# Optimization experiments

Measured on AMD Instinct MI355X. Metric: run time of the kernel, lower is better.

## Reference

```python
import jax, jax.numpy as jnp
import numpy as np

D_MODEL = 512
D_STATE = 16
D_CONV = 5
EXPAND = 2
HEADDIM = 64
D_INNER = EXPAND * D_MODEL            # 1024
NHEADS = D_INNER // HEADDIM           # 16
NGROUPS = 1
CONV_DIM = D_INNER + 2 * NGROUPS * D_STATE          # 1056
D_IN_PROJ = 2 * D_INNER + 2 * NGROUPS * D_STATE + NHEADS  # 2096
B_SZ, SEQ = 16, 960
EPS = 1e-5


def _mamba_params(key):
    ks = jax.random.split(key, 5)
    return dict(
        W_in=jax.random.normal(ks[0], (D_MODEL, D_IN_PROJ), jnp.float32) * 0.02,
        conv_w=jax.random.normal(ks[1], (CONV_DIM, D_CONV), jnp.float32) * 0.1,
        conv_b=jnp.zeros((CONV_DIM,), jnp.float32),
        dt_bias=jnp.log(jnp.expm1(jax.random.uniform(ks[2], (NHEADS,), jnp.float32, 0.001, 0.1))),
        A_log=jnp.log(jax.random.uniform(ks[3], (NHEADS,), jnp.float32, 1.0, 16.0)),
        D=jnp.ones((NHEADS,), jnp.float32),
        norm_w=jnp.ones((D_INNER,), jnp.float32),
        W_out=jax.random.normal(ks[4], (D_INNER, D_MODEL), jnp.float32) * 0.02,
    )


def setup_inputs() -> dict:
    key = jax.random.key(0)
    kx, kf, kb, kp = jax.random.split(key, 4)
    inp = {"x": jax.random.normal(kx, (B_SZ, SEQ, D_MODEL), jnp.float32)}
    for pref, k in (("fwd_", kf), ("bwd_", kb)):
        for n, v in _mamba_params(k).items():
            inp[pref + n] = v
    kp1, kp2 = jax.random.split(kp)
    inp["proj_W"] = jax.random.normal(kp1, (2 * D_MODEL, D_MODEL), jnp.float32) * 0.02
    inp["proj_b"] = jnp.zeros((D_MODEL,), jnp.float32)
    inp["ln_g"] = jnp.ones((D_MODEL,), jnp.float32)
    inp["ln_b"] = jnp.zeros((D_MODEL,), jnp.float32)
    return inp


def _mamba2(x, W_in, conv_w, conv_b, dt_bias, A_log, D, norm_w, W_out):
    """Mamba-2 block (mamba_ssm semantics): in_proj -> causal depthwise conv
    + silu -> selective SSM scan -> gated RMSNorm -> out_proj."""
    B, L, _ = x.shape
    zxbcdt = x @ W_in                                  # (B,L,2096)
    z = zxbcdt[..., :D_INNER]
    xBC = zxbcdt[..., D_INNER:D_INNER + CONV_DIM]
    dt = jax.nn.softplus(zxbcdt[..., D_INNER + CONV_DIM:] + dt_bias)  # (B,L,H)
    # causal depthwise conv over time
    xp = jnp.pad(xBC, ((0, 0), (D_CONV - 1, 0), (0, 0))).transpose(0, 2, 1)  # (B,C,Lp)
    xc = jax.lax.conv_general_dilated(
        xp, conv_w[:, None, :], window_strides=(1,), padding='VALID',
        dimension_numbers=('NCH', 'OIH', 'NCH'),
        feature_group_count=CONV_DIM).transpose(0, 2, 1)                  # (B,L,C)
    xBC = jax.nn.silu(xc + conv_b)
    xs = xBC[..., :D_INNER].reshape(B, L, NHEADS, HEADDIM)                # (B,L,H,P)
    Bm = xBC[..., D_INNER:D_INNER + D_STATE]                              # (B,L,N)
    Cm = xBC[..., D_INNER + D_STATE:]                                     # (B,L,N)
    A = -jnp.exp(A_log)                                                   # (H,)
    dA = jnp.exp(dt * A)                                                  # (B,L,H)
    dtx = dt[..., None] * xs                                              # (B,L,H,P)

    def step(h, inp):
        dA_t, dtx_t, B_t, C_t = inp
        # h: (B,H,P,N)
        h = h * dA_t[:, :, None, None] + jnp.einsum('bhp,bn->bhpn', dtx_t, B_t)
        y = jnp.einsum('bhpn,bn->bhp', h, C_t)
        return h, y

    h0 = jnp.zeros((B, NHEADS, HEADDIM, D_STATE), x.dtype)
    _, ys = jax.lax.scan(
        step, h0,
        (dA.transpose(1, 0, 2), dtx.transpose(1, 0, 2, 3),
         Bm.transpose(1, 0, 2), Cm.transpose(1, 0, 2)))
    y = ys.transpose(1, 0, 2, 3) + D[None, None, :, None] * xs            # (B,L,H,P)
    y = y.reshape(B, L, D_INNER)
    # gated RMSNorm (norm_before_gate=False)
    y = y * jax.nn.silu(z)
    y = y * jax.lax.rsqrt(jnp.mean(y * y, axis=-1, keepdims=True) + EPS) * norm_w
    return y @ W_out


def reference(x,
              fwd_W_in, fwd_conv_w, fwd_conv_b, fwd_dt_bias, fwd_A_log, fwd_D, fwd_norm_w, fwd_W_out,
              bwd_W_in, bwd_conv_w, bwd_conv_b, bwd_dt_bias, bwd_A_log, bwd_D, bwd_norm_w, bwd_W_out,
              proj_W, proj_b, ln_g, ln_b):
    x_f = _mamba2(x, fwd_W_in, fwd_conv_w, fwd_conv_b, fwd_dt_bias, fwd_A_log, fwd_D, fwd_norm_w, fwd_W_out)
    x_b = jnp.flip(_mamba2(jnp.flip(x, 1), bwd_W_in, bwd_conv_w, bwd_conv_b, bwd_dt_bias, bwd_A_log, bwd_D, bwd_norm_w, bwd_W_out), 1)
    x_out = jnp.concatenate([x_f, x_b], axis=-1) @ proj_W + proj_b
    h = x + x_out  # dropout is identity in eval
    mu = jnp.mean(h, axis=-1, keepdims=True)
    var = jnp.mean((h - mu) ** 2, axis=-1, keepdims=True)
    return (h - mu) * jax.lax.rsqrt(var + EPS) * ln_g + ln_b
```

## Files before the change

kernel.cpp:

```cpp
#include <hip/hip_runtime.h>
#include <hip/hip_bf16.h>

#define D_MODEL   512
#define D_STATE   16
#define D_CONV    5
#define HEADDIM   64
#define D_INNER   1024
#define NHEADS    16
#define CONV_DIM  1056
#define D_IN_PROJ 2096
#define B_SZ      16
#define SEQ       960
#define MROWS     (B_SZ*SEQ)
#define EPS       1e-5f
#define NCHUNK    6
#define CLEN      160

typedef __attribute__((ext_vector_type(8))) short   short8;
typedef __attribute__((ext_vector_type(8))) ushort  u16x8;
typedef __attribute__((ext_vector_type(4))) float   f32x4;

__device__ __forceinline__ ushort bf16_rne(float f) {
  union { float f; unsigned u; } x; x.f = f;
  unsigned u = x.u;
  return (ushort)((u + 0x7FFFu + ((u >> 16) & 1u)) >> 16);
}
__device__ __forceinline__ float bf16_f(ushort h) {
  union { unsigned u; float f; } x; x.u = ((unsigned)h) << 16;
  return x.f;
}
__device__ __forceinline__ void cvt_split(float v, ushort& h, ushort& l) {
  h = bf16_rne(v);
  l = bf16_rne(v - bf16_f(h));
}

#define LDK 40

__global__ __launch_bounds__(256) void gemm_mfma(
    const float* __restrict__ A, const float* __restrict__ Bt,
    float* __restrict__ C, const float* __restrict__ bias,
    int M, int N, int K, int lda, int ldb, int ldc, int accum)
{
  __shared__ ushort As_hi[128][LDK], As_lo[128][LDK];
  __shared__ ushort Bs_hi[128][LDK], Bs_lo[128][LDK];

  const int tid  = threadIdx.x;
  const int lane = tid & 63;
  const int wave = tid >> 6;
  const int wm   = wave >> 1;
  const int wn   = wave & 1;
  const int brow = blockIdx.x * 128;
  const int bcol = blockIdx.y * 128;

  const int sr = tid >> 1;
  const int sq = (tid & 1) * 16;

  f32x4 acc[4][4];
  #pragma unroll
  for (int i = 0; i < 4; ++i)
    #pragma unroll
    for (int j = 0; j < 4; ++j) acc[i][j] = f32x4{0.f, 0.f, 0.f, 0.f};

  const int fr = lane & 15;
  const int fk = (lane >> 4) * 8;

#define CS(F, HV, LV, I) { ushort th_, tl_; cvt_split((F), th_, tl_); HV[I] = th_; LV[I] = tl_; }

  for (int k0 = 0; k0 < K; k0 += 32) {
    {
      const float* s = &A[(size_t)(brow + sr) * lda + k0 + sq];
      float4 a0 = *(const float4*)(s);
      float4 a1 = *(const float4*)(s + 4);
      float4 a2 = *(const float4*)(s + 8);
      float4 a3 = *(const float4*)(s + 12);
      u16x8 h0, h1, l0, l1;
      CS(a0.x, h0, l0, 0) CS(a0.y, h0, l0, 1) CS(a0.z, h0, l0, 2) CS(a0.w, h0, l0, 3)
      CS(a1.x, h0, l0, 4) CS(a1.y, h0, l0, 5) CS(a1.z, h0, l0, 6) CS(a1.w, h0, l0, 7)
      CS(a2.x, h1, l1, 0) CS(a2.y, h1, l1, 1) CS(a2.z, h1, l1, 2) CS(a2.w, h1, l1, 3)
      CS(a3.x, h1, l1, 4) CS(a3.y, h1, l1, 5) CS(a3.z, h1, l1, 6) CS(a3.w, h1, l1, 7)
      *(u16x8*)&As_hi[sr][sq]     = h0;
      *(u16x8*)&As_hi[sr][sq + 8] = h1;
      *(u16x8*)&As_lo[sr][sq]     = l0;
      *(u16x8*)&As_lo[sr][sq + 8] = l1;
    }
    {
      int n = bcol + sr;
      u16x8 h0 = {0,0,0,0,0,0,0,0}, h1 = h0, l0 = h0, l1 = h0;
      if (n < N) {
        const float* s = &Bt[(size_t)n * ldb + k0 + sq];
        float4 b0 = *(const float4*)(s);
        float4 b1 = *(const float4*)(s + 4);
        float4 b2 = *(const float4*)(s + 8);
        float4 b3 = *(const float4*)(s + 12);
        CS(b0.x, h0, l0, 0) CS(b0.y, h0, l0, 1) CS(b0.z, h0, l0, 2) CS(b0.w, h0, l0, 3)
        CS(b1.x, h0, l0, 4) CS(b1.y, h0, l0, 5) CS(b1.z, h0, l0, 6) CS(b1.w, h0, l0, 7)
        CS(b2.x, h1, l1, 0) CS(b2.y, h1, l1, 1) CS(b2.z, h1, l1, 2) CS(b2.w, h1, l1, 3)
        CS(b3.x, h1, l1, 4) CS(b3.y, h1, l1, 5) CS(b3.z, h1, l1, 6) CS(b3.w, h1, l1, 7)
      }
      *(u16x8*)&Bs_hi[sr][sq]     = h0;
      *(u16x8*)&Bs_hi[sr][sq + 8] = h1;
      *(u16x8*)&Bs_lo[sr][sq]     = l0;
      *(u16x8*)&Bs_lo[sr][sq + 8] = l1;
    }
    __syncthreads();

    short8 ah[4], al[4], bh[4], bl[4];
    #pragma unroll
    for (int mf = 0; mf < 4; ++mf) {
      int r = wm * 64 + mf * 16 + fr;
      ah[mf] = *(const short8*)&As_hi[r][fk];
      al[mf] = *(const short8*)&As_lo[r][fk];
    }
    #pragma unroll
    for (int nf = 0; nf < 4; ++nf) {
      int n = wn * 64 + nf * 16 + fr;
      bh[nf] = *(const short8*)&Bs_hi[n][fk];
      bl[nf] = *(const short8*)&Bs_lo[n][fk];
    }
    #pragma unroll
    for (int mf = 0; mf < 4; ++mf)
      #pragma unroll
      for (int nf = 0; nf < 4; ++nf) {
        acc[mf][nf] = __builtin_amdgcn_mfma_f32_16x16x32_bf16(ah[mf], bh[nf], acc[mf][nf], 0, 0, 0);
        acc[mf][nf] = __builtin_amdgcn_mfma_f32_16x16x32_bf16(ah[mf], bl[nf], acc[mf][nf], 0, 0, 0);
        acc[mf][nf] = __builtin_amdgcn_mfma_f32_16x16x32_bf16(al[mf], bh[nf], acc[mf][nf], 0, 0, 0);
      }
    __syncthreads();
  }
#undef CS

  const int orow0 = brow + wm * 64 + ((lane >> 4) << 2);
  const int ocol0 = bcol + wn * 64 + fr;
  #pragma unroll
  for (int nf = 0; nf < 4; ++nf) {
    int col = ocol0 + nf * 16;
    if (col < N) {
      float bv = bias ? bias[col] : 0.f;
      #pragma unroll
      for (int mf = 0; mf < 4; ++mf) {
        #pragma unroll
        for (int j = 0; j < 4; ++j) {
          size_t idx = (size_t)(orow0 + mf * 16 + j) * ldc + col;
          float v = acc[mf][nf][j] + bv;
          if (accum) v += C[idx];
          C[idx] = v;
        }
      }
    }
  }
}

__global__ __launch_bounds__(256) void transpose_f32(
    const float* __restrict__ in, float* __restrict__ out, int R, int C)
{
  __shared__ float t[32][33];
  int c0 = blockIdx.x * 32, r0 = blockIdx.y * 32;
  int tx = threadIdx.x & 31, ty = threadIdx.x >> 5;
  #pragma unroll
  for (int i = 0; i < 32; i += 8) {
    int r = r0 + ty + i, c = c0 + tx;
    t[ty + i][tx] = (r < R && c < C) ? in[(size_t)r * C + c] : 0.f;
  }
  __syncthreads();
  #pragma unroll
  for (int i = 0; i < 32; i += 8) {
    int c = c0 + ty + i, r = r0 + tx;
    if (c < C && r < R) out[(size_t)c * R + r] = t[tx][ty + i];
  }
}

#define BM 128
#define BN 128
#define BKK 16

__global__ __launch_bounds__(256) void gemm_f32(
    const float* __restrict__ A, const float* __restrict__ B,
    float* __restrict__ C, const float* __restrict__ bias,
    int N, int K, int lda, int ldb, int ldc, int accum)
{
  __shared__ float As[BKK][BM + 4];
  __shared__ float Bs[BKK][BN + 4];

  const int tid = threadIdx.x;
  const int bm = blockIdx.x * BM;
  const int bn = blockIdx.y * BN;
  const int tx = tid & 15;
  const int ty = tid >> 4;

  const int am = tid >> 2;
  const int ak = (tid & 3) * 4;
  const int bk = tid >> 5;
  const int bc = (tid & 31) * 4;

  float acc[8][8];
  #pragma unroll
  for (int i = 0; i < 8; ++i)
    #pragma unroll
    for (int j = 0; j < 8; ++j) acc[i][j] = 0.f;

  const int colb = bn + bc;
  const bool bok = (colb < N);

  for (int k0 = 0; k0 < K; k0 += BKK) {
    float4 av0 = *(const float4*)&A[(size_t)(bm + am) * lda + k0 + ak];
    float4 av1 = *(const float4*)&A[(size_t)(bm + am + 64) * lda + k0 + ak];
    As[ak + 0][am]      = av0.x; As[ak + 1][am]      = av0.y;
    As[ak + 2][am]      = av0.z; As[ak + 3][am]      = av0.w;
    As[ak + 0][am + 64] = av1.x; As[ak + 1][am + 64] = av1.y;
    As[ak + 2][am + 64] = av1.z; As[ak + 3][am + 64] = av1.w;
    float4 z4 = make_float4(0.f, 0.f, 0.f, 0.f);
    float4 bv0 = bok ? *(const float4*)&B[(size_t)(k0 + bk) * ldb + colb]     : z4;
    float4 bv1 = bok ? *(const float4*)&B[(size_t)(k0 + bk + 8) * ldb + colb] : z4;
    *(float4*)&Bs[bk][bc]     = bv0;
    *(float4*)&Bs[bk + 8][bc] = bv1;
    __syncthreads();

    #pragma unroll
    for (int k = 0; k < BKK; ++k) {
      float4 a0 = *(const float4*)&As[k][ty * 4];
      float4 a1 = *(const float4*)&As[k][64 + ty * 4];
      float4 b0 = *(const float4*)&Bs[k][tx * 4];
      float4 b1 = *(const float4*)&Bs[k][64 + tx * 4];
      float a[8] = {a0.x, a0.y, a0.z, a0.w, a1.x, a1.y, a1.z, a1.w};
      float bb[8] = {b0.x, b0.y, b0.z, b0.w, b1.x, b1.y, b1.z, b1.w};
      #pragma unroll
      for (int i = 0; i < 8; ++i)
        #pragma unroll
        for (int j = 0; j < 8; ++j)
          acc[i][j] = __builtin_fmaf(a[i], bb[j], acc[i][j]);
    }
    __syncthreads();
  }

  const int n0 = bn + tx * 4;
  const int n1 = bn + 64 + tx * 4;
  float4 bias0 = make_float4(0.f, 0.f, 0.f, 0.f), bias1 = bias0;
  if (bias) {
    if (n0 < N) bias0 = *(const float4*)&bias[n0];
    if (n1 < N) bias1 = *(const float4*)&bias[n1];
  }
  #pragma unroll
  for (int i = 0; i < 8; ++i) {
    int row = bm + ((i < 4) ? (ty * 4 + i) : (64 + ty * 4 + i - 4));
    if (n0 < N) {
      float4 v = make_float4(acc[i][0] + bias0.x, acc[i][1] + bias0.y,
                             acc[i][2] + bias0.z, acc[i][3] + bias0.w);
      if (accum) {
        float4 c = *(const float4*)&C[(size_t)row * ldc + n0];
        v.x += c.x; v.y += c.y; v.z += c.z; v.w += c.w;
      }
      *(float4*)&C[(size_t)row * ldc + n0] = v;
    }
    if (n1 < N) {
      float4 v = make_float4(acc[i][4] + bias1.x, acc[i][5] + bias1.y,
                             acc[i][6] + bias1.z, acc[i][7] + bias1.w);
      if (accum) {
        float4 c = *(const float4*)&C[(size_t)row * ldc + n1];
        v.x += c.x; v.y += c.y; v.z += c.z; v.w += c.w;
      }
      *(float4*)&C[(size_t)row * ldc + n1] = v;
    }
  }
}

__global__ __launch_bounds__(256) void conv_silu(
    const float* __restrict__ zx, const float* __restrict__ cw,
    const float* __restrict__ cb, float* __restrict__ out, int dir)
{
  int idx = blockIdx.x * 256 + threadIdx.x;
  if (idx >= MROWS * CONV_DIM) return;
  int c  = idx % CONV_DIM;
  int bl = idx / CONV_DIM;
  int l  = bl % SEQ;
  int rowbase = bl - l;

  float acc = 0.f;
  #pragma unroll
  for (int j = 0; j < D_CONV; ++j) {
    int li = dir ? (l + 4 - j) : (l - 4 + j);
    if (li >= 0 && li < SEQ)
      acc = __builtin_fmaf(cw[c * D_CONV + j],
                           zx[(size_t)(rowbase + li) * D_IN_PROJ + D_INNER + c], acc);
  }
  float v = acc + cb[c];
  out[idx] = v / (1.f + __expf(-v));
}

__global__ __launch_bounds__(64) void scan_pass1(
    const float* __restrict__ zx, const float* __restrict__ xc,
    const float* __restrict__ dtb_p, const float* __restrict__ Alog_p,
    float* __restrict__ states, float* __restrict__ Pbuf, int dir)
{
  int blk = blockIdx.x;
  int c   = blk % NCHUNK;
  int bh  = blk / NCHUNK;
  int b = bh >> 4, hd = bh & 15;
  float dtb = dtb_p[hd];
  float A   = -__expf(Alog_p[hd]);
  int p = threadIdx.x;
  const float* xrow = xc + (size_t)b * SEQ * CONV_DIM;
  const float* zrow = zx + (size_t)b * SEQ * D_IN_PROJ;

  float h[16];
  #pragma unroll
  for (int n = 0; n < 16; ++n) h[n] = 0.f;
  float P = 1.f;

  const int s0 = c * CLEN, s1 = s0 + CLEN;

  float xv0, dtr0; float4 B0[4];
  float xv1, dtr1; float4 B1[4];

#define P1LOAD(ss, XV, DTR, BB) do {                                        \
    int tt_ = dir ? (SEQ - 1 - (ss)) : (ss);                                \
    size_t xb_ = (size_t)tt_ * CONV_DIM;                                    \
    XV  = xrow[xb_ + hd * 64 + p];                                          \
    DTR = zrow[(size_t)tt_ * D_IN_PROJ + (D_INNER + CONV_DIM) + hd];        \
    const float4* B4_ = (const float4*)(xrow + xb_ + D_INNER);              \
    BB[0] = B4_[0]; BB[1] = B4_[1]; BB[2] = B4_[2]; BB[3] = B4_[3];         \
  } while (0)

  P1LOAD(s0, xv0, dtr0, B0);
  P1LOAD(s0 + 1, xv1, dtr1, B1);

  #pragma unroll 4
  for (int s = s0; s < s1; ++s) {
    float dtrb = dtr0 + dtb;
    float dt = (dtrb > 20.f) ? dtrb : log1pf(__expf(dtrb));
    float dA = __expf(dt * A);
    P *= dA;
    float dtx = dt * xv0;
#define ST1(n, Bc) h[n] = __builtin_fmaf(h[n], dA, dtx * (Bc));
    ST1(0,  B0[0].x) ST1(1,  B0[0].y) ST1(2,  B0[0].z) ST1(3,  B0[0].w)
    ST1(4,  B0[1].x) ST1(5,  B0[1].y) ST1(6,  B0[1].z) ST1(7,  B0[1].w)
    ST1(8,  B0[2].x) ST1(9,  B0[2].y) ST1(10, B0[2].z) ST1(11, B0[2].w)
    ST1(12, B0[3].x) ST1(13, B0[3].y) ST1(14, B0[3].z) ST1(15, B0[3].w)
#undef ST1
    xv0 = xv1; dtr0 = dtr1;
    #pragma unroll
    for (int q = 0; q < 4; ++q) B0[q] = B1[q];
    int sn = s + 2; if (sn > s1 - 1) sn = s1 - 1;
    P1LOAD(sn, xv1, dtr1, B1);
  }
#undef P1LOAD

  float4* sp = (float4*)&states[(((size_t)bh * NCHUNK + c) * 64 + p) * 16];
  sp[0] = make_float4(h[0],  h[1],  h[2],  h[3]);
  sp[1] = make_float4(h[4],  h[5],  h[6],  h[7]);
  sp[2] = make_float4(h[8],  h[9],  h[10], h[11]);
  sp[3] = make_float4(h[12], h[13], h[14], h[15]);
  if (p == 0) Pbuf[bh * NCHUNK + c] = P;
}

__global__ __launch_bounds__(64) void scan_combine(
    float* __restrict__ states, const float* __restrict__ Pbuf)
{
  int bh = blockIdx.x;
  int p  = threadIdx.x;
  float4 h0 = make_float4(0,0,0,0), h1 = h0, h2 = h0, h3 = h0;
  for (int c = 0; c < NCHUNK; ++c) {
    float4* sp = (float4*)&states[(((size_t)bh * NCHUNK + c) * 64 + p) * 16];
    float P = Pbuf[bh * NCHUNK + c];
    float4 s0 = sp[0], s1 = sp[1], s2 = sp[2], s3 = sp[3];
    sp[0] = h0; sp[1] = h1; sp[2] = h2; sp[3] = h3;
    h0.x = __builtin_fmaf(P, h0.x, s0.x); h0.y = __builtin_fmaf(P, h0.y, s0.y);
    h0.z = __builtin_fmaf(P, h0.z, s0.z); h0.w = __builtin_fmaf(P, h0.w, s0.w);
    h1.x = __builtin_fmaf(P, h1.x, s1.x); h1.y = __builtin_fmaf(P, h1.y, s1.y);
    h1.z = __builtin_fmaf(P, h1.z, s1.z); h1.w = __builtin_fmaf(P, h1.w, s1.w);
    h2.x = __builtin_fmaf(P, h2.x, s2.x); h2.y = __builtin_fmaf(P, h2.y, s2.y);
    h2.z = __builtin_fmaf(P, h2.z, s2.z); h2.w = __builtin_fmaf(P, h2.w, s2.w);
    h3.x = __builtin_fmaf(P, h3.x, s3.x); h3.y = __builtin_fmaf(P, h3.y, s3.y);
    h3.z = __builtin_fmaf(P, h3.z, s3.z); h3.w = __builtin_fmaf(P, h3.w, s3.w);
  }
}

__global__ __launch_bounds__(64) void scan_pass3(
    const float* __restrict__ zx, const float* __restrict__ xc,
    const float* __restrict__ dtb_p, const float* __restrict__ Alog_p,
    const float* __restrict__ D_p, const float* __restrict__ states,
    float* __restrict__ y, int dir)
{
  int blk = blockIdx.x;
  int c   = blk % NCHUNK;
  int bh  = blk / NCHUNK;
  int b = bh >> 4, hd = bh & 15;
  float dtb = dtb_p[hd];
  float A   = -__expf(Alog_p[hd]);
  float Dv  = D_p[hd];
  int p = threadIdx.x;
  const float* xrow = xc + (size_t)b * SEQ * CONV_DIM;
  const float* zrow = zx + (size_t)b * SEQ * D_IN_PROJ;
  float*       yrow = y  + (size_t)b * SEQ * D_IN_PROJ + hd * 64 + p;

  float h[16];
  {
    const float4* sp =
        (const float4*)&states[(((size_t)bh * NCHUNK + c) * 64 + p) * 16];
    float4 s0 = sp[0], s1 = sp[1], s2 = sp[2], s3 = sp[3];
    h[0]=s0.x; h[1]=s0.y; h[2]=s0.z; h[3]=s0.w;
    h[4]=s1.x; h[5]=s1.y; h[6]=s1.z; h[7]=s1.w;
    h[8]=s2.x; h[9]=s2.y; h[10]=s2.z; h[11]=s2.w;
    h[12]=s3.x; h[13]=s3.y; h[14]=s3.z; h[15]=s3.w;
  }

  const int s0i = c * CLEN, s1i = s0i + CLEN;

  float xv0, zv0, dtr0; float4 B0[4], C0[4];
  float xv1, zv1, dtr1; float4 B1[4], C1[4];

#define P3LOAD(ss, XV, ZV, DTR, BB, CC) do {                                \
    int tt_ = dir ? (SEQ - 1 - (ss)) : (ss);                                \
    size_t xb_ = (size_t)tt_ * CONV_DIM;                                    \
    size_t zb_ = (size_t)tt_ * D_IN_PROJ;                                   \
    XV  = xrow[xb_ + hd * 64 + p];                                          \
    ZV  = zrow[zb_ + hd * 64 + p];                                          \
    DTR = zrow[zb_ + (D_INNER + CONV_DIM) + hd];                            \
    const float4* B4_ = (const float4*)(xrow + xb_ + D_INNER);              \
    const float4* C4_ = (const float4*)(xrow + xb_ + D_INNER + D_STATE);    \
    BB[0] = B4_[0]; BB[1] = B4_[1]; BB[2] = B4_[2]; BB[3] = B4_[3];         \
    CC[0] = C4_[0]; CC[1] = C4_[1]; CC[2] = C4_[2]; CC[3] = C4_[3];         \
  } while (0)

  P3LOAD(s0i, xv0, zv0, dtr0, B0, C0);
  P3LOAD(s0i + 1, xv1, zv1, dtr1, B1, C1);

  #pragma unroll 4
  for (int s = s0i; s < s1i; ++s) {
    int tt = dir ? (SEQ - 1 - s) : s;
    float dtrb = dtr0 + dtb;
    float dt = (dtrb > 20.f) ? dtrb : log1pf(__expf(dtrb));
    float dA = __expf(dt * A);
    float dtx = dt * xv0;
    float yv = 0.f;
#define ST3(n, Bc, Cc) \
    h[n] = __builtin_fmaf(h[n], dA, dtx * (Bc)); \
    yv = __builtin_fmaf(h[n], (Cc), yv);
    ST3(0,  B0[0].x, C0[0].x) ST3(1,  B0[0].y, C0[0].y)
    ST3(2,  B0[0].z, C0[0].z) ST3(3,  B0[0].w, C0[0].w)
    ST3(4,  B0[1].x, C0[1].x) ST3(5,  B0[1].y, C0[1].y)
    ST3(6,  B0[1].z, C0[1].z) ST3(7,  B0[1].w, C0[1].w)
    ST3(8,  B0[2].x, C0[2].x) ST3(9,  B0[2].y, C0[2].y)
    ST3(10, B0[2].z, C0[2].z) ST3(11, B0[2].w, C0[2].w)
    ST3(12, B0[3].x, C0[3].x) ST3(13, B0[3].y, C0[3].y)
    ST3(14, B0[3].z, C0[3].z) ST3(15, B0[3].w, C0[3].w)
#undef ST3

    float sz = zv0 / (1.f + __expf(-zv0));
    yrow[(size_t)tt * D_IN_PROJ] = (yv + Dv * xv0) * sz;

    xv0 = xv1; zv0 = zv1; dtr0 = dtr1;
    #pragma unroll
    for (int q = 0; q < 4; ++q) { B0[q] = B1[q]; C0[q] = C1[q]; }
    int sn = s + 2; if (sn > s1i - 1) sn = s1i - 1;
    P3LOAD(sn, xv1, zv1, dtr1, B1, C1);
  }
#undef P3LOAD
}

__device__ __forceinline__ float wave_sum64(float v) {
  #pragma unroll
  for (int off = 32; off; off >>= 1) v += __shfl_xor(v, off, 64);
  return v;
}

__global__ __launch_bounds__(256) void rmsnorm_kernel(
    float* __restrict__ y, const float* __restrict__ w, int ld)
{
  int row = blockIdx.x;
  float4* yp = (float4*)(y + (size_t)row * ld);
  int c = threadIdx.x;
  float4 v = yp[c];
  float ss = v.x * v.x + v.y * v.y + v.z * v.z + v.w * v.w;
  ss = wave_sum64(ss);
  __shared__ float part[4];
  if ((threadIdx.x & 63) == 0) part[threadIdx.x >> 6] = ss;
  __syncthreads();
  float tot = part[0] + part[1] + part[2] + part[3];
  float scale = rsqrtf(tot * (1.f / D_INNER) + EPS);
  float4 wv = ((const float4*)w)[c];
  v.x *= scale * wv.x; v.y *= scale * wv.y;
  v.z *= scale * wv.z; v.w *= scale * wv.w;
  yp[c] = v;
}

__global__ __launch_bounds__(256) void ln_final(
    const float* __restrict__ x, const float* __restrict__ xo,
    const float* __restrict__ g, const float* __restrict__ bb,
    float* __restrict__ out)
{
  int row = blockIdx.x;
  int c = threadIdx.x;
  float2 xv = ((const float2*)(x  + (size_t)row * D_MODEL))[c];
  float2 ov = ((const float2*)(xo + (size_t)row * D_MODEL))[c];
  float hx = xv.x + ov.x, hy = xv.y + ov.y;
  float s  = hx + hy;
  float sq = hx * hx + hy * hy;
  s  = wave_sum64(s);
  sq = wave_sum64(sq);
  __shared__ float ps[4], pq[4];
  if ((threadIdx.x & 63) == 0) { ps[threadIdx.x >> 6] = s; pq[threadIdx.x >> 6] = sq; }
  __syncthreads();
  float tots = ps[0] + ps[1] + ps[2] + ps[3];
  float totq = pq[0] + pq[1] + pq[2] + pq[3];
  float mu  = tots * (1.f / D_MODEL);
  float var = totq * (1.f / D_MODEL) - mu * mu;
  float inv = rsqrtf(var + EPS);
  float2 gv = ((const float2*)g)[c];
  float2 bv = ((const float2*)bb)[c];
  float2 o;
  o.x = (hx - mu) * inv * gv.x + bv.x;
  o.y = (hy - mu) * inv * gv.y + bv.y;
  ((float2*)(out + (size_t)row * D_MODEL))[c] = o;
}

extern "C" void kernel_launch(void* const* d_in, const int* in_sizes, int n_in,
                              void* d_out, int out_size, void* d_ws, size_t ws_size,
                              hipStream_t stream) {
  const float* x      = (const float*)d_in[0];
  const float* proj_W = (const float*)d_in[17];
  const float* proj_b = (const float*)d_in[18];
  const float* ln_g   = (const float*)d_in[19];
  const float* ln_b   = (const float*)d_in[20];
  float* out = (float*)d_out;

  const size_t SZ_Z  = (size_t)MROWS * D_IN_PROJ;
  const size_t SZ_C  = (size_t)MROWS * CONV_DIM;
  const size_t SZ_W  = (size_t)D_INNER * D_MODEL;
  const size_t SZ_ST = (size_t)256 * NCHUNK * 64 * 16;
  const size_t SZ_P  = (size_t)256 * NCHUNK;
  const size_t SZ_SH = (SZ_ST + SZ_P > SZ_W) ? (SZ_ST + SZ_P) : SZ_W;
  const size_t NEED  = (SZ_Z + SZ_C + SZ_SH) * sizeof(float);
  if (ws_size < NEED) {
    hipMemsetAsync(d_out, 0, (size_t)out_size * sizeof(float), stream);
    return;
  }
  float* zbuf    = (float*)d_ws;
  float* convbuf = zbuf + SZ_Z;
  float* shared  = convbuf + SZ_C;
  float* WinT    = shared;
  float* states  = shared;
  float* Pbuf    = shared + SZ_ST;
  float* Wcomb   = shared;
  float* WcombT  = shared + SZ_W;
  float* ybuf    = zbuf + D_INNER;

  dim3 blk(256);

  for (int dir = 0; dir < 2; ++dir) {
    const float* W_in    = (const float*)d_in[dir ? 9  : 1];
    const float* conv_w  = (const float*)d_in[dir ? 10 : 2];
    const float* conv_b  = (const float*)d_in[dir ? 11 : 3];
    const float* dt_bias = (const float*)d_in[dir ? 12 : 4];
    const float* A_log   = (const float*)d_in[dir ? 13 : 5];
    const float* Dp      = (const float*)d_in[dir ? 14 : 6];
    const float* norm_w  = (const float*)d_in[dir ? 15 : 7];
    const float* W_out   = (const float*)d_in[dir ? 16 : 8];

    transpose_f32<<<dim3(66, 16), blk, 0, stream>>>(W_in, WinT, D_MODEL, D_IN_PROJ);

    gemm_mfma<<<dim3(MROWS / 128, 17), blk, 0, stream>>>(
        x, WinT, zbuf, nullptr,
        MROWS, D_IN_PROJ, D_MODEL, D_MODEL, D_MODEL, D_IN_PROJ, 0);

    {
      dim3 grid((MROWS * CONV_DIM + 255) / 256);
      conv_silu<<<grid, blk, 0, stream>>>(zbuf, conv_w, conv_b, convbuf, dir);
    }
    scan_pass1<<<dim3(256 * NCHUNK), dim3(64), 0, stream>>>(
        zbuf, convbuf, dt_bias, A_log, states, Pbuf, dir);
    scan_combine<<<dim3(256), dim3(64), 0, stream>>>(states, Pbuf);
    scan_pass3<<<dim3(256 * NCHUNK), dim3(64), 0, stream>>>(
        zbuf, convbuf, dt_bias, A_log, Dp, states, ybuf, dir);
    rmsnorm_kernel<<<dim3(MROWS), blk, 0, stream>>>(ybuf, norm_w, D_IN_PROJ);
    {
      dim3 grid(D_INNER / BM, (D_MODEL + BN - 1) / BN);
      gemm_f32<<<grid, blk, 0, stream>>>(
          W_out, proj_W + (size_t)dir * D_MODEL * D_MODEL, Wcomb, nullptr,
          D_MODEL, D_MODEL, D_MODEL, D_MODEL, D_MODEL, 0);
      transpose_f32<<<dim3(16, 32), blk, 0, stream>>>(Wcomb, WcombT, D_INNER, D_MODEL);
    }
    gemm_mfma<<<dim3(MROWS / 128, 4), blk, 0, stream>>>(
        ybuf, WcombT, out, dir ? nullptr : proj_b,
        MROWS, D_MODEL, D_INNER, D_IN_PROJ, D_INNER, D_MODEL, dir);
  }

  ln_final<<<dim3(MROWS), blk, 0, stream>>>(x, out, ln_g, ln_b, out);
}
```

Baseline: 1.350 ms.

## Pre-split operands into bf16 hi/lo buffers once instead of per GEMM tile

New measurement: 1.348 ms. No clear change (-0.2%).

```diff
diff --git a/kernel.cpp b/kernel.cpp
--- a/kernel.cpp
+++ b/kernel.cpp
@@ -18,6 +18,7 @@
 
 typedef __attribute__((ext_vector_type(8))) short   short8;
 typedef __attribute__((ext_vector_type(8))) ushort  u16x8;
+typedef __attribute__((ext_vector_type(4))) ushort  u16x4;
 typedef __attribute__((ext_vector_type(4))) float   f32x4;
 
 __device__ __forceinline__ ushort bf16_rne(float f) {
@@ -33,11 +34,55 @@
   h = bf16_rne(v);
   l = bf16_rne(v - bf16_f(h));
 }
+#define CVT_SPLIT_V(F, HV, LV, I) do { ushort th_, tl_; \
+    cvt_split((F), th_, tl_); HV[I] = th_; LV[I] = tl_; } while (0)
+
+__global__ __launch_bounds__(256) void split_f32(
+    const float* __restrict__ in, ushort* __restrict__ hi,
+    ushort* __restrict__ lo, int n4)
+{
+  int i = blockIdx.x * 256 + threadIdx.x;
+  if (i >= n4) return;
+  float4 v = ((const float4*)in)[i];
+  u16x4 h, l;
+  CVT_SPLIT_V(v.x, h, l, 0);
+  CVT_SPLIT_V(v.y, h, l, 1);
+  CVT_SPLIT_V(v.z, h, l, 2);
+  CVT_SPLIT_V(v.w, h, l, 3);
+  ((u16x4*)hi)[i] = h;
+  ((u16x4*)lo)[i] = l;
+}
+
+__global__ __launch_bounds__(256) void transpose_split(
+    const float* __restrict__ in, ushort* __restrict__ oh,
+    ushort* __restrict__ ol, int R, int C)
+{
+  __shared__ float t[32][33];
+  int c0 = blockIdx.x * 32, r0 = blockIdx.y * 32;
+  int tx = threadIdx.x & 31, ty = threadIdx.x >> 5;
+  #pragma unroll
+  for (int i = 0; i < 32; i += 8) {
+    int r = r0 + ty + i, c = c0 + tx;
+    t[ty + i][tx] = (r < R && c < C) ? in[(size_t)r * C + c] : 0.f;
+  }
+  __syncthreads();
+  #pragma unroll
+  for (int i = 0; i < 32; i += 8) {
+    int c = c0 + ty + i, r = r0 + tx;
+    if (c < C && r < R) {
+      ushort h, l;
+      cvt_split(t[tx][ty + i], h, l);
+      oh[(size_t)c * R + r] = h;
+      ol[(size_t)c * R + r] = l;
+    }
+  }
+}
 
 #define LDK 40
 
-__global__ __launch_bounds__(256) void gemm_mfma(
-    const float* __restrict__ A, const float* __restrict__ Bt,
+__global__ __launch_bounds__(256) void gemm_mfma_bf16(
+    const ushort* __restrict__ Ah, const ushort* __restrict__ Al,
+    const ushort* __restrict__ Bth, const ushort* __restrict__ Btl,
     float* __restrict__ C, const float* __restrict__ bias,
     int M, int N, int K, int lda, int ldb, int ldc, int accum)
 {
@@ -64,38 +109,24 @@
   const int fr = lane & 15;
   const int fk = (lane >> 4) * 8;
 
-#define CS(F, HV, LV, I) { ushort th_, tl_; cvt_split((F), th_, tl_); HV[I] = th_; LV[I] = tl_; }
-
   for (int k0 = 0; k0 < K; k0 += 32) {
     {
-      const float* s = &A[(size_t)(brow + sr) * lda + k0 + sq];
-      float4 a0 = *(const float4*)(s);
-      float4 a1 = *(const float4*)(s + 4);
-      float4 a2 = *(const float4*)(s + 8);
-      float4 a3 = *(const float4*)(s + 12);
-      u16x8 h0, h1, l0, l1;
-      CS(a0.x, h0, l0, 0) CS(a0.y, h0, l0, 1) CS(a0.z, h0, l0, 2) CS(a0.w, h0, l0, 3)
-      CS(a1.x, h0, l0, 4) CS(a1.y, h0, l0, 5) CS(a1.z, h0, l0, 6) CS(a1.w, h0, l0, 7)
-      CS(a2.x, h1, l1, 0) CS(a2.y, h1, l1, 1) CS(a2.z, h1, l1, 2) CS(a2.w, h1, l1, 3)
-      CS(a3.x, h1, l1, 4) CS(a3.y, h1, l1, 5) CS(a3.z, h1, l1, 6) CS(a3.w, h1, l1, 7)
-      *(u16x8*)&As_hi[sr][sq]     = h0;
-      *(u16x8*)&As_hi[sr][sq + 8] = h1;
-      *(u16x8*)&As_lo[sr][sq]     = l0;
-      *(u16x8*)&As_lo[sr][sq + 8] = l1;
+      size_t off = (size_t)(brow + sr) * lda + k0 + sq;
+      *(u16x8*)&As_hi[sr][sq]     = *(const u16x8*)&Ah[off];
+      *(u16x8*)&As_hi[sr][sq + 8] = *(const u16x8*)&Ah[off + 8];
+      *(u16x8*)&As_lo[sr][sq]     = *(const u16x8*)&Al[off];
+      *(u16x8*)&As_lo[sr][sq + 8] = *(const u16x8*)&Al[off + 8];
     }
     {
       int n = bcol + sr;
-      u16x8 h0 = {0,0,0,0,0,0,0,0}, h1 = h0, l0 = h0, l1 = h0;
+      u16x8 z8 = {0,0,0,0,0,0,0,0};
+      u16x8 h0 = z8, h1 = z8, l0 = z8, l1 = z8;
       if (n < N) {
-        const float* s = &Bt[(size_t)n * ldb + k0 + sq];
-        float4 b0 = *(const float4*)(s);
-        float4 b1 = *(const float4*)(s + 4);
-        float4 b2 = *(const float4*)(s + 8);
-        float4 b3 = *(const float4*)(s + 12);
-        CS(b0.x, h0, l0, 0) CS(b0.y, h0, l0, 1) CS(b0.z, h0, l0, 2) CS(b0.w, h0, l0, 3)
-        CS(b1.x, h0, l0, 4) CS(b1.y, h0, l0, 5) CS(b1.z, h0, l0, 6) CS(b1.w, h0, l0, 7)
-        CS(b2.x, h1, l1, 0) CS(b2.y, h1, l1, 1) CS(b2.z, h1, l1, 2) CS(b2.w, h1, l1, 3)
-        CS(b3.x, h1, l1, 4) CS(b3.y, h1, l1, 5) CS(b3.z, h1, l1, 6) CS(b3.w, h1, l1, 7)
+        size_t off = (size_t)n * ldb + k0 + sq;
+        h0 = *(const u16x8*)&Bth[off];
+        h1 = *(const u16x8*)&Bth[off + 8];
+        l0 = *(const u16x8*)&Btl[off];
+        l1 = *(const u16x8*)&Btl[off + 8];
       }
       *(u16x8*)&Bs_hi[sr][sq]     = h0;
       *(u16x8*)&Bs_hi[sr][sq + 8] = h1;
@@ -127,7 +158,6 @@
       }
     __syncthreads();
   }
-#undef CS
 
   const int orow0 = brow + wm * 64 + ((lane >> 4) << 2);
   const int ocol0 = bcol + wn * 64 + fr;
@@ -147,25 +177,6 @@
         }
       }
     }
-  }
-}
-
-__global__ __launch_bounds__(256) void transpose_f32(
-    const float* __restrict__ in, float* __restrict__ out, int R, int C)
-{
-  __shared__ float t[32][33];
-  int c0 = blockIdx.x * 32, r0 = blockIdx.y * 32;
-  int tx = threadIdx.x & 31, ty = threadIdx.x >> 5;
-  #pragma unroll
-  for (int i = 0; i < 32; i += 8) {
-    int r = r0 + ty + i, c = c0 + tx;
-    t[ty + i][tx] = (r < R && c < C) ? in[(size_t)r * C + c] : 0.f;
-  }
-  __syncthreads();
-  #pragma unroll
-  for (int i = 0; i < 32; i += 8) {
-    int c = c0 + ty + i, r = r0 + tx;
-    if (c < C && r < R) out[(size_t)c * R + r] = t[tx][ty + i];
   }
 }
 
@@ -463,11 +474,12 @@
   return v;
 }
 
-__global__ __launch_bounds__(256) void rmsnorm_kernel(
-    float* __restrict__ y, const float* __restrict__ w, int ld)
+__global__ __launch_bounds__(256) void rmsnorm_split(
+    const float* __restrict__ y, const float* __restrict__ w,
+    ushort* __restrict__ yh, ushort* __restrict__ yl)
 {
   int row = blockIdx.x;
-  float4* yp = (float4*)(y + (size_t)row * ld);
+  const float4* yp = (const float4*)(y + (size_t)row * D_IN_PROJ);
   int c = threadIdx.x;
   float4 v = yp[c];
   float ss = v.x * v.x + v.y * v.y + v.z * v.z + v.w * v.w;
@@ -478,9 +490,13 @@
   float tot = part[0] + part[1] + part[2] + part[3];
   float scale = rsqrtf(tot * (1.f / D_INNER) + EPS);
   float4 wv = ((const float4*)w)[c];
-  v.x *= scale * wv.x; v.y *= scale * wv.y;
-  v.z *= scale * wv.z; v.w *= scale * wv.w;
-  yp[c] = v;
+  u16x4 h, l;
+  CVT_SPLIT_V(v.x * scale * wv.x, h, l, 0);
+  CVT_SPLIT_V(v.y * scale * wv.y, h, l, 1);
+  CVT_SPLIT_V(v.z * scale * wv.z, h, l, 2);
+  CVT_SPLIT_V(v.w * scale * wv.w, h, l, 3);
+  ((u16x4*)(yh + (size_t)row * D_INNER))[c] = h;
+  ((u16x4*)(yl + (size_t)row * D_INNER))[c] = l;
 }
 
 __global__ __launch_bounds__(256) void ln_final(
@@ -531,18 +547,25 @@
   const size_t SZ_SH = (SZ_ST + SZ_P > SZ_W) ? (SZ_ST + SZ_P) : SZ_W;
   const size_t NEED  = (SZ_Z + SZ_C + SZ_SH) * sizeof(float);
   if (ws_size < NEED) {
-    hipMemsetAsync(d_out, 0, (size_t)out_size * sizeof(float), stream);
+    (void)hipMemsetAsync(d_out, 0, (size_t)out_size * sizeof(float), stream);
     return;
   }
   float* zbuf    = (float*)d_ws;
   float* convbuf = zbuf + SZ_Z;
   float* shared  = convbuf + SZ_C;
-  float* WinT    = shared;
   float* states  = shared;
   float* Pbuf    = shared + SZ_ST;
-  float* Wcomb   = shared;
-  float* WcombT  = shared + SZ_W;
   float* ybuf    = zbuf + D_INNER;
+
+  ushort* x_hi    = (ushort*)convbuf;
+  ushort* x_lo    = x_hi + (size_t)MROWS * D_MODEL;
+  ushort* WinT_hi = x_lo + (size_t)MROWS * D_MODEL;
+  ushort* WinT_lo = WinT_hi + (size_t)D_IN_PROJ * D_MODEL;
+  ushort* y_hi    = (ushort*)convbuf;
+  ushort* y_lo    = y_hi + (size_t)MROWS * D_INNER;
+  float*  Wcomb   = shared;
+  ushort* WcT_hi  = (ushort*)(shared + SZ_W);
+  ushort* WcT_lo  = WcT_hi + (size_t)D_MODEL * D_INNER;
 
   dim3 blk(256);
 
@@ -556,10 +579,15 @@
     const float* norm_w  = (const float*)d_in[dir ? 15 : 7];
     const float* W_out   = (const float*)d_in[dir ? 16 : 8];
 
-    transpose_f32<<<dim3(66, 16), blk, 0, stream>>>(W_in, WinT, D_MODEL, D_IN_PROJ);
-
-    gemm_mfma<<<dim3(MROWS / 128, 17), blk, 0, stream>>>(
-        x, WinT, zbuf, nullptr,
+    {
+      int n4 = MROWS * D_MODEL / 4;
+      split_f32<<<dim3((n4 + 255) / 256), blk, 0, stream>>>(x, x_hi, x_lo, n4);
+    }
+    transpose_split<<<dim3(66, 16), blk, 0, stream>>>(
+        W_in, WinT_hi, WinT_lo, D_MODEL, D_IN_PROJ);
+
+    gemm_mfma_bf16<<<dim3(MROWS / 128, 17), blk, 0, stream>>>(
+        x_hi, x_lo, WinT_hi, WinT_lo, zbuf, nullptr,
         MROWS, D_IN_PROJ, D_MODEL, D_MODEL, D_MODEL, D_IN_PROJ, 0);
 
     {
@@ -571,17 +599,18 @@
     scan_combine<<<dim3(256), dim3(64), 0, stream>>>(states, Pbuf);
     scan_pass3<<<dim3(256 * NCHUNK), dim3(64), 0, stream>>>(
         zbuf, convbuf, dt_bias, A_log, Dp, states, ybuf, dir);
-    rmsnorm_kernel<<<dim3(MROWS), blk, 0, stream>>>(ybuf, norm_w, D_IN_PROJ);
+    rmsnorm_split<<<dim3(MROWS), blk, 0, stream>>>(ybuf, norm_w, y_hi, y_lo);
     {
       dim3 grid(D_INNER / BM, (D_MODEL + BN - 1) / BN);
       gemm_f32<<<grid, blk, 0, stream>>>(
           W_out, proj_W + (size_t)dir * D_MODEL * D_MODEL, Wcomb, nullptr,
           D_MODEL, D_MODEL, D_MODEL, D_MODEL, D_MODEL, 0);
-      transpose_f32<<<dim3(16, 32), blk, 0, stream>>>(Wcomb, WcombT, D_INNER, D_MODEL);
-    }
-    gemm_mfma<<<dim3(MROWS / 128, 4), blk, 0, stream>>>(
-        ybuf, WcombT, out, dir ? nullptr : proj_b,
-        MROWS, D_MODEL, D_INNER, D_IN_PROJ, D_INNER, D_MODEL, dir);
+      transpose_split<<<dim3(16, 32), blk, 0, stream>>>(
+          Wcomb, WcT_hi, WcT_lo, D_INNER, D_MODEL);
+    }
+    gemm_mfma_bf16<<<dim3(MROWS / 128, 4), blk, 0, stream>>>(
+        y_hi, y_lo, WcT_hi, WcT_lo, out, dir ? nullptr : proj_b,
+        MROWS, D_MODEL, D_INNER, D_INNER, D_INNER, D_MODEL, dir);
   }
 
   ln_final<<<dim3(MROWS), blk, 0, stream>>>(x, out, ln_g, ln_b, out);
```
